# Kernel tuning notes

Hardware: AMD Instinct MI355X
Metric: run time of the kernel (lower is better)

Reference implementation:

```python
import jax, jax.numpy as jnp
import numpy as np

NUM_HEADS = 16
NUM_KV_HEADS = 8
HEAD_DIM = 128
SCALE = 1.0 / np.sqrt(HEAD_DIM)  # 0.08838834764831845
SEQ_LENS = [1536, 512, 1024, 1024]  # ragged packed sequences, total T=4096


def setup_inputs() -> dict:
    key = jax.random.key(0)
    k1, k2, k3 = jax.random.split(key, 3)
    T = sum(SEQ_LENS)
    q = jax.random.normal(k1, (T, NUM_HEADS * HEAD_DIM), dtype=jnp.float32)
    k = jax.random.normal(k2, (T, NUM_KV_HEADS * HEAD_DIM), dtype=jnp.float32)
    v = jax.random.normal(k3, (T, NUM_KV_HEADS * HEAD_DIM), dtype=jnp.float32)
    # positions restart at 0 for each packed sequence; jumps mark boundaries
    positions = jnp.asarray(np.concatenate([np.arange(L) for L in SEQ_LENS]), dtype=jnp.int32)
    return {"q": q, "k": k, "v": v, "positions": positions}


def reference(q, k, v, positions):
    T = q.shape[0]
    G = NUM_HEADS // NUM_KV_HEADS  # GQA group size
    qh = q.reshape(T, NUM_KV_HEADS, G, HEAD_DIM)
    kh = k.reshape(T, NUM_KV_HEADS, HEAD_DIM)
    vh = v.reshape(T, NUM_KV_HEADS, HEAD_DIM)
    # segment ids from position jumps (positions[i] != positions[i-1] + 1)
    jump = jnp.concatenate([
        jnp.zeros((1,), jnp.int32),
        (positions[1:] != positions[:-1] + 1).astype(jnp.int32),
    ])
    seg = jnp.cumsum(jump)  # [T]
    idx = jnp.arange(T)
    # attend only within the same packed sequence, causally
    mask = (seg[:, None] == seg[None, :]) & (idx[:, None] >= idx[None, :])  # [T, T]
    # scores: [kv_head, group, T_q, T_k]
    scores = jnp.einsum('tkgd,skd->kgts', qh, kh) * jnp.float32(SCALE)
    scores = jnp.where(mask[None, None], scores, jnp.float32(-1e30))
    p = jax.nn.softmax(scores, axis=-1)
    o = jnp.einsum('kgts,skd->tkgd', p, vh)
    return o.reshape(T, NUM_HEADS * HEAD_DIM)
```

## Files before the change

kernel.cpp:

```cpp
#include <hip/hip_runtime.h>
#include <cstdint>
#include <cstddef>

#define NUM_KV   8
#define GQA      2
#define HD       128
#define QSTRIDE  2048
#define KSTRIDE  1024
#define SCALE_LOG2E 0.12751741032075463f

typedef float    f32x4  __attribute__((ext_vector_type(4)));
typedef float    f32x2  __attribute__((ext_vector_type(2)));
typedef float    f32x16 __attribute__((ext_vector_type(16)));
typedef unsigned u32x4  __attribute__((ext_vector_type(4)));
typedef __bf16   bf16x8 __attribute__((ext_vector_type(8)));
typedef __bf16   bf16x2 __attribute__((ext_vector_type(2)));

union U8 { unsigned short u[8]; unsigned d[4]; u32x4 q; bf16x8 v; };

__device__ __forceinline__ unsigned short f2b(float f) {
    union { float f; unsigned u; } x;
    x.f = f;
    unsigned r = x.u + 0x7fffu + ((x.u >> 16) & 1u);
    return (unsigned short)(r >> 16);
}
__device__ __forceinline__ unsigned pkb(float x, float y) {
    f32x2 f = {x, y};
    bf16x2 b = __builtin_convertvector(f, bf16x2);
    union { bf16x2 b; unsigned u; } c; c.b = b;
    return c.u;
}

#define PS_STRIDE 40

__global__ __launch_bounds__(512)
void swizzle_k(const float* __restrict__ kg, unsigned short* __restrict__ Kswz,
               int T, int NT)
{
    const int tt = blockIdx.x, h = blockIdx.y;
    const int tid = threadIdx.x;
    const int c = tid >> 6, lane = tid & 63;
    const int col = lane & 31, hk = lane >> 5;
    const int row = min(tt * 32 + col, T - 1);
    const float* src = kg + (size_t)row * KSTRIDE + h * HD + c * 16 + hk * 8;
    f32x4 a = ((const f32x4*)src)[0];
    f32x4 b = ((const f32x4*)src)[1];
    u32x4 W;
    W[0] = pkb(a[0], a[1]); W[1] = pkb(a[2], a[3]);
    W[2] = pkb(b[0], b[1]); W[3] = pkb(b[2], b[3]);
    *(u32x4*)(Kswz + (((size_t)h * NT + tt) * 8 + c) * 512 + lane * 8) = W;
}

__global__ __launch_bounds__(512)
void swizzle_v(const float* __restrict__ vg, unsigned short* __restrict__ Vswz,
               int T, int NT)
{
    const int tt = blockIdx.x, h = blockIdx.y;
    const int tid = threadIdx.x;
    const int f = tid >> 6, lane = tid & 63;
    const int col = lane & 31, hk = lane >> 5;
    const int d  = (f >> 1) * 32 + col;
    const int r0 = tt * 32 + (f & 1) * 16 + hk * 8;
    float x[8];
#pragma unroll
    for (int j = 0; j < 8; ++j) {
        const int row = min(r0 + j, T - 1);
        x[j] = vg[(size_t)row * KSTRIDE + h * HD + d];
    }
    u32x4 W;
    W[0] = pkb(x[0], x[1]); W[1] = pkb(x[2], x[3]);
    W[2] = pkb(x[4], x[5]); W[3] = pkb(x[6], x[7]);
    *(u32x4*)(Vswz + (((size_t)h * NT + tt) * 8 + f) * 512 + lane * 8) = W;
}

__global__ __launch_bounds__(256, 2)
void attn_kernel(const float* __restrict__ qg, const unsigned short* __restrict__ Kswz,
                 const unsigned short* __restrict__ Vswz, const int* __restrict__ pos,
                 float* __restrict__ out, int T, int NT)
{
    __shared__ __align__(16) float Obuf[4][32 * 128];
    __shared__ float Lb[4][32];
    __shared__ __align__(16) unsigned short Ps[4][32 * PS_STRIDE];

    const int tid  = threadIdx.x;
    const int w    = tid >> 6;
    const int lane = tid & 63;
    const int col  = lane & 31;
    const int hk   = lane >> 5;

    const int bid = blockIdx.x;
    const int kvh = bid & 7;
    const int g   = (bid >> 3) & 1;
    const int qtr = bid >> 4;
    const int nq  = (T + 31) >> 5;
    const int qt  = nq - 1 - qtr;
    const int row0 = qt * 32;
    if (row0 >= T) return;
    const int hq = kvh * GQA + g;

    const int kend = min(row0 + 32, T);
    const int k_lo = row0 - pos[row0];

    const int rbase = row0 + 4 * hk;
    int rstart[16];
#pragma unroll
    for (int r = 0; r < 16; ++r) {
        const int rg = rbase + (r & 3) + 8 * (r >> 2);
        const int rc = min(rg, T - 1);
        rstart[r] = rc - pos[rc];
    }
    int rs_max = rstart[0];
#pragma unroll
    for (int r = 1; r < 16; ++r) rs_max = max(rs_max, rstart[r]);
    rs_max = max(rs_max, __shfl_xor(rs_max, 32));

    bf16x8 qf[8];
    {
        const int qr = min(row0 + col, T - 1);
        const float* qp = qg + (size_t)qr * QSTRIDE + hq * HD + hk * 8;
#pragma unroll
        for (int c = 0; c < 8; ++c) {
            f32x4 f0 = ((const f32x4*)(qp + c * 16))[0];
            f32x4 f1 = ((const f32x4*)(qp + c * 16))[1];
            U8 u;
            u.d[0] = pkb(f0[0] * SCALE_LOG2E, f0[1] * SCALE_LOG2E);
            u.d[1] = pkb(f0[2] * SCALE_LOG2E, f0[3] * SCALE_LOG2E);
            u.d[2] = pkb(f1[0] * SCALE_LOG2E, f1[1] * SCALE_LOG2E);
            u.d[3] = pkb(f1[2] * SCALE_LOG2E, f1[3] * SCALE_LOG2E);
            qf[c] = u.v;
        }
    }

    f32x16 acc[4];
#pragma unroll
    for (int nt = 0; nt < 4; ++nt)
#pragma unroll
        for (int r = 0; r < 16; ++r) acc[nt][r] = 0.f;
    float l_vec[16];
#pragma unroll
    for (int r = 0; r < 16; ++r) l_vec[r] = 0.f;

    const int t_lo = k_lo >> 5;
    const int t_hi = (kend + 31) >> 5;
    const unsigned short* kb_base = Kswz + (size_t)kvh * NT * 4096;
    const unsigned short* vb_base = Vswz + (size_t)kvh * NT * 4096;

    U8 kf[8], kfn[8], vf[8];
    int tt = t_lo + w;
    if (tt < t_hi) {
        const unsigned short* kp = kb_base + (size_t)tt * 4096 + lane * 8;
#pragma unroll
        for (int c = 0; c < 8; ++c) kf[c].q = *(const u32x4*)(kp + c * 512);
    }

    for (; tt < t_hi; tt += 4) {
        const int ttn = tt + 4;
        if (ttn < t_hi) {
            const unsigned short* kp = kb_base + (size_t)ttn * 4096 + lane * 8;
#pragma unroll
            for (int c = 0; c < 8; ++c) kfn[c].q = *(const u32x4*)(kp + c * 512);
        }
        {
            const unsigned short* vp = vb_base + (size_t)tt * 4096 + lane * 8;
#pragma unroll
            for (int f = 0; f < 8; ++f) vf[f].q = *(const u32x4*)(vp + f * 512);
        }

        f32x16 s;
#pragma unroll
        for (int r = 0; r < 16; ++r) s[r] = 0.f;
#pragma unroll
        for (int c = 0; c < 8; ++c)
            s = __builtin_amdgcn_mfma_f32_32x32x16_bf16(qf[c], kf[c].v, s, 0, 0, 0);

        const int kb  = tt * 32;
        const int key = kb + col;
        float p[16];
        if (kb >= rs_max && kb + 32 <= row0 + 1) {
#pragma unroll
            for (int r = 0; r < 16; ++r) { p[r] = exp2f(s[r]); l_vec[r] += p[r]; }
        } else {
#pragma unroll
            for (int r = 0; r < 16; ++r) {
                const int rg = rbase + (r & 3) + 8 * (r >> 2);
                const float x = (key >= rstart[r] && key <= rg) ? s[r] : -3e38f;
                p[r] = exp2f(x);
                l_vec[r] += p[r];
            }
        }

        unsigned short* Pw = (unsigned short*)Ps[w];
#pragma unroll
        for (int r = 0; r < 16; ++r)
            Pw[((r & 3) + 8 * (r >> 2) + 4 * hk) * PS_STRIDE + col] = f2b(p[r]);
        U8 pa0, pa1;
        pa0.q = *(const u32x4*)&Pw[col * PS_STRIDE + hk * 8];
        pa1.q = *(const u32x4*)&Pw[col * PS_STRIDE + 16 + hk * 8];

#pragma unroll
        for (int nt = 0; nt < 4; ++nt) {
            acc[nt] = __builtin_amdgcn_mfma_f32_32x32x16_bf16(pa0.v, vf[nt * 2].v,     acc[nt], 0, 0, 0);
            acc[nt] = __builtin_amdgcn_mfma_f32_32x32x16_bf16(pa1.v, vf[nt * 2 + 1].v, acc[nt], 0, 0, 0);
        }
#pragma unroll
        for (int c = 0; c < 8; ++c) kf[c] = kfn[c];
    }

#pragma unroll
    for (int r = 0; r < 16; ++r) {
        float sl = l_vec[r];
        sl += __shfl_xor(sl, 1);
        sl += __shfl_xor(sl, 2);
        sl += __shfl_xor(sl, 4);
        sl += __shfl_xor(sl, 8);
        sl += __shfl_xor(sl, 16);
        if (col == 0) Lb[w][(r & 3) + 8 * (r >> 2) + 4 * hk] = sl;
    }
#pragma unroll
    for (int nt = 0; nt < 4; ++nt)
#pragma unroll
        for (int r = 0; r < 16; ++r)
            Obuf[w][((r & 3) + 8 * (r >> 2) + 4 * hk) * 128 + nt * 32 + col] = acc[nt][r];

    __syncthreads();

    const int orow = tid >> 3;
    const int oc   = (tid & 7) * 16;
    const int rg   = row0 + orow;
    const float lsum = Lb[0][orow] + Lb[1][orow] + Lb[2][orow] + Lb[3][orow];
    const float inv  = (lsum > 0.f) ? (1.0f / lsum) : 0.f;
    if (rg < T) {
        float* op = out + (size_t)rg * QSTRIDE + hq * HD + oc;
#pragma unroll
        for (int j = 0; j < 4; ++j) {
            f32x4 sv = *(const f32x4*)&Obuf[0][orow * 128 + oc + j * 4];
#pragma unroll
            for (int ww = 1; ww < 4; ++ww) {
                f32x4 t = *(const f32x4*)&Obuf[ww][orow * 128 + oc + j * 4];
                sv[0] += t[0]; sv[1] += t[1]; sv[2] += t[2]; sv[3] += t[3];
            }
            sv[0] *= inv; sv[1] *= inv; sv[2] *= inv; sv[3] *= inv;
            *(f32x4*)(op + j * 4) = sv;
        }
    }
}

extern "C" void kernel_launch(void* const* d_in, const int* in_sizes, int n_in,
                              void* d_out, int out_size, void* d_ws, size_t ws_size,
                              hipStream_t stream) {
    const float* q   = (const float*)d_in[0];
    const float* k   = (const float*)d_in[1];
    const float* v   = (const float*)d_in[2];
    const int*   pos = (const int*)d_in[3];
    float* out = (float*)d_out;
    const int T  = in_sizes[0] / QSTRIDE;
    const int NT = (T + 31) / 32;

    unsigned short* Kswz = (unsigned short*)d_ws;
    unsigned short* Vswz = Kswz + (size_t)NUM_KV * NT * 4096;

    swizzle_k<<<dim3(NT, NUM_KV), 512, 0, stream>>>(k, Kswz, T, NT);
    swizzle_v<<<dim3(NT, NUM_KV), 512, 0, stream>>>(v, Vswz, T, NT);

    attn_kernel<<<dim3(NT * 16), 256, 0, stream>>>(q, Kswz, Vswz, pos, out, T, NT);
}
```

Baseline: 170.2 us.

## Fuse K/V swizzle kernels, compute S transposed, shuffle P in registers, shrink LDS

```diff
diff --git a/kernel.cpp b/kernel.cpp
--- a/kernel.cpp
+++ b/kernel.cpp
@@ -15,15 +15,10 @@
 typedef unsigned u32x4  __attribute__((ext_vector_type(4)));
 typedef __bf16   bf16x8 __attribute__((ext_vector_type(8)));
 typedef __bf16   bf16x2 __attribute__((ext_vector_type(2)));
+typedef int      i32x2  __attribute__((ext_vector_type(2)));
 
 union U8 { unsigned short u[8]; unsigned d[4]; u32x4 q; bf16x8 v; };
 
-__device__ __forceinline__ unsigned short f2b(float f) {
-    union { float f; unsigned u; } x;
-    x.f = f;
-    unsigned r = x.u + 0x7fffu + ((x.u >> 16) & 1u);
-    return (unsigned short)(r >> 16);
-}
 __device__ __forceinline__ unsigned pkb(float x, float y) {
     f32x2 f = {x, y};
     bf16x2 b = __builtin_convertvector(f, bf16x2);
@@ -31,56 +26,56 @@
     return c.u;
 }
 
-#define PS_STRIDE 40
+__device__ __forceinline__ void pl32swap(unsigned &a, unsigned &b) {
+    i32x2 r = __builtin_amdgcn_permlane32_swap((int)a, (int)b, false, false);
+    a = (unsigned)r[0];
+    b = (unsigned)r[1];
+}
 
 __global__ __launch_bounds__(512)
-void swizzle_k(const float* __restrict__ kg, unsigned short* __restrict__ Kswz,
-               int T, int NT)
-{
-    const int tt = blockIdx.x, h = blockIdx.y;
-    const int tid = threadIdx.x;
-    const int c = tid >> 6, lane = tid & 63;
-    const int col = lane & 31, hk = lane >> 5;
-    const int row = min(tt * 32 + col, T - 1);
-    const float* src = kg + (size_t)row * KSTRIDE + h * HD + c * 16 + hk * 8;
-    f32x4 a = ((const f32x4*)src)[0];
-    f32x4 b = ((const f32x4*)src)[1];
-    u32x4 W;
-    W[0] = pkb(a[0], a[1]); W[1] = pkb(a[2], a[3]);
-    W[2] = pkb(b[0], b[1]); W[3] = pkb(b[2], b[3]);
-    *(u32x4*)(Kswz + (((size_t)h * NT + tt) * 8 + c) * 512 + lane * 8) = W;
-}
-
-__global__ __launch_bounds__(512)
-void swizzle_v(const float* __restrict__ vg, unsigned short* __restrict__ Vswz,
-               int T, int NT)
+void swizzle_kv(const float* __restrict__ kg, const float* __restrict__ vg,
+                unsigned short* __restrict__ Kswz, unsigned short* __restrict__ Vswz,
+                int T, int NT)
 {
     const int tt = blockIdx.x, h = blockIdx.y;
     const int tid = threadIdx.x;
     const int f = tid >> 6, lane = tid & 63;
     const int col = lane & 31, hk = lane >> 5;
-    const int d  = (f >> 1) * 32 + col;
-    const int r0 = tt * 32 + (f & 1) * 16 + hk * 8;
-    float x[8];
-#pragma unroll
-    for (int j = 0; j < 8; ++j) {
-        const int row = min(r0 + j, T - 1);
-        x[j] = vg[(size_t)row * KSTRIDE + h * HD + d];
-    }
-    u32x4 W;
-    W[0] = pkb(x[0], x[1]); W[1] = pkb(x[2], x[3]);
-    W[2] = pkb(x[4], x[5]); W[3] = pkb(x[6], x[7]);
-    *(u32x4*)(Vswz + (((size_t)h * NT + tt) * 8 + f) * 512 + lane * 8) = W;
-}
-
-__global__ __launch_bounds__(256, 2)
+
+    if (blockIdx.z == 0) {
+        const int row = min(tt * 32 + col, T - 1);
+        const float* src = kg + (size_t)row * KSTRIDE + h * HD + f * 16 + hk * 8;
+        f32x4 a = ((const f32x4*)src)[0];
+        f32x4 b = ((const f32x4*)src)[1];
+        u32x4 W;
+        W[0] = pkb(a[0], a[1]); W[1] = pkb(a[2], a[3]);
+        W[2] = pkb(b[0], b[1]); W[3] = pkb(b[2], b[3]);
+        *(u32x4*)(Kswz + (((size_t)h * NT + tt) * 8 + f) * 512 + lane * 8) = W;
+    } else {
+        const int d  = (f >> 1) * 32 + col;
+        const int r0 = tt * 32 + (f & 1) * 16 + hk * 8;
+        float x[8];
+#pragma unroll
+        for (int j = 0; j < 8; ++j) {
+            const int row = min(r0 + j, T - 1);
+            x[j] = vg[(size_t)row * KSTRIDE + h * HD + d];
+        }
+        u32x4 W;
+        W[0] = pkb(x[0], x[1]); W[1] = pkb(x[2], x[3]);
+        W[2] = pkb(x[4], x[5]); W[3] = pkb(x[6], x[7]);
+        *(u32x4*)(Vswz + (((size_t)h * NT + tt) * 8 + f) * 512 + lane * 8) = W;
+    }
+}
+
+#define OB_STRIDE 132
+
+__global__ __launch_bounds__(256, 4)
 void attn_kernel(const float* __restrict__ qg, const unsigned short* __restrict__ Kswz,
                  const unsigned short* __restrict__ Vswz, const int* __restrict__ pos,
                  float* __restrict__ out, int T, int NT)
 {
-    __shared__ __align__(16) float Obuf[4][32 * 128];
-    __shared__ float Lb[4][32];
-    __shared__ __align__(16) unsigned short Ps[4][32 * PS_STRIDE];
+    __shared__ __align__(16) float Obuf[32 * OB_STRIDE];
+    __shared__ float Lb[32];
 
     const int tid  = threadIdx.x;
     const int w    = tid >> 6;
@@ -98,21 +93,21 @@
     if (row0 >= T) return;
     const int hq = kvh * GQA + g;
 
+    for (int i = tid; i < 32 * OB_STRIDE; i += 256) Obuf[i] = 0.f;
+    if (tid < 32) Lb[tid] = 0.f;
+    __syncthreads();
+
     const int kend = min(row0 + 32, T);
     const int k_lo = row0 - pos[row0];
 
-    const int rbase = row0 + 4 * hk;
-    int rstart[16];
-#pragma unroll
-    for (int r = 0; r < 16; ++r) {
-        const int rg = rbase + (r & 3) + 8 * (r >> 2);
-        const int rc = min(rg, T - 1);
-        rstart[r] = rc - pos[rc];
-    }
-    int rs_max = rstart[0];
-#pragma unroll
-    for (int r = 1; r < 16; ++r) rs_max = max(rs_max, rstart[r]);
-    rs_max = max(rs_max, __shfl_xor(rs_max, 32));
+    const int qrow   = min(row0 + col, T - 1);
+    const int rstart = qrow - pos[qrow];
+    int rs_max = rstart;
+    rs_max = max(rs_max, __shfl_xor(rs_max, 1));
+    rs_max = max(rs_max, __shfl_xor(rs_max, 2));
+    rs_max = max(rs_max, __shfl_xor(rs_max, 4));
+    rs_max = max(rs_max, __shfl_xor(rs_max, 8));
+    rs_max = max(rs_max, __shfl_xor(rs_max, 16));
 
     bf16x8 qf[8];
     {
@@ -136,9 +131,7 @@
     for (int nt = 0; nt < 4; ++nt)
 #pragma unroll
         for (int r = 0; r < 16; ++r) acc[nt][r] = 0.f;
-    float l_vec[16];
-#pragma unroll
-    for (int r = 0; r < 16; ++r) l_vec[r] = 0.f;
+    float l_lane = 0.f;
 
     const int t_lo = k_lo >> 5;
     const int t_hi = (kend + 31) >> 5;
@@ -169,76 +162,72 @@
         f32x16 s;
 #pragma unroll
         for (int r = 0; r < 16; ++r) s[r] = 0.f;
+        __builtin_amdgcn_s_setprio(1);
 #pragma unroll
         for (int c = 0; c < 8; ++c)
-            s = __builtin_amdgcn_mfma_f32_32x32x16_bf16(qf[c], kf[c].v, s, 0, 0, 0);
-
-        const int kb  = tt * 32;
-        const int key = kb + col;
+            s = __builtin_amdgcn_mfma_f32_32x32x16_bf16(kf[c].v, qf[c], s, 0, 0, 0);
+        __builtin_amdgcn_s_setprio(0);
+
+        const int kb = tt * 32;
         float p[16];
         if (kb >= rs_max && kb + 32 <= row0 + 1) {
 #pragma unroll
-            for (int r = 0; r < 16; ++r) { p[r] = exp2f(s[r]); l_vec[r] += p[r]; }
+            for (int r = 0; r < 16; ++r) { p[r] = exp2f(s[r]); l_lane += p[r]; }
         } else {
 #pragma unroll
             for (int r = 0; r < 16; ++r) {
-                const int rg = rbase + (r & 3) + 8 * (r >> 2);
-                const float x = (key >= rstart[r] && key <= rg) ? s[r] : -3e38f;
+                const int key = kb + (r & 3) + 8 * (r >> 2) + 4 * hk;
+                const float x = (key >= rstart && key <= qrow) ? s[r] : -3e38f;
                 p[r] = exp2f(x);
-                l_vec[r] += p[r];
+                l_lane += p[r];
             }
         }
 
-        unsigned short* Pw = (unsigned short*)Ps[w];
-#pragma unroll
-        for (int r = 0; r < 16; ++r)
-            Pw[((r & 3) + 8 * (r >> 2) + 4 * hk) * PS_STRIDE + col] = f2b(p[r]);
+        unsigned a0 = pkb(p[0],  p[1]),  a1 = pkb(p[2],  p[3]);
+        unsigned b0 = pkb(p[4],  p[5]),  b1 = pkb(p[6],  p[7]);
+        pl32swap(a0, b0); pl32swap(a1, b1);
+        unsigned c0 = pkb(p[8],  p[9]),  c1 = pkb(p[10], p[11]);
+        unsigned d0 = pkb(p[12], p[13]), d1 = pkb(p[14], p[15]);
+        pl32swap(c0, d0); pl32swap(c1, d1);
         U8 pa0, pa1;
-        pa0.q = *(const u32x4*)&Pw[col * PS_STRIDE + hk * 8];
-        pa1.q = *(const u32x4*)&Pw[col * PS_STRIDE + 16 + hk * 8];
-
+        pa0.d[0] = a0; pa0.d[1] = a1; pa0.d[2] = b0; pa0.d[3] = b1;
+        pa1.d[0] = c0; pa1.d[1] = c1; pa1.d[2] = d0; pa1.d[3] = d1;
+
+        __builtin_amdgcn_s_setprio(1);
 #pragma unroll
         for (int nt = 0; nt < 4; ++nt) {
             acc[nt] = __builtin_amdgcn_mfma_f32_32x32x16_bf16(pa0.v, vf[nt * 2].v,     acc[nt], 0, 0, 0);
             acc[nt] = __builtin_amdgcn_mfma_f32_32x32x16_bf16(pa1.v, vf[nt * 2 + 1].v, acc[nt], 0, 0, 0);
         }
+        __builtin_amdgcn_s_setprio(0);
+
 #pragma unroll
         for (int c = 0; c < 8; ++c) kf[c] = kfn[c];
     }
 
-#pragma unroll
-    for (int r = 0; r < 16; ++r) {
-        float sl = l_vec[r];
-        sl += __shfl_xor(sl, 1);
-        sl += __shfl_xor(sl, 2);
-        sl += __shfl_xor(sl, 4);
-        sl += __shfl_xor(sl, 8);
-        sl += __shfl_xor(sl, 16);
-        if (col == 0) Lb[w][(r & 3) + 8 * (r >> 2) + 4 * hk] = sl;
+    {
+        const float ls = l_lane + __shfl_xor(l_lane, 32);
+        if (hk == 0) atomicAdd(&Lb[col], ls);
     }
 #pragma unroll
     for (int nt = 0; nt < 4; ++nt)
 #pragma unroll
         for (int r = 0; r < 16; ++r)
-            Obuf[w][((r & 3) + 8 * (r >> 2) + 4 * hk) * 128 + nt * 32 + col] = acc[nt][r];
+            atomicAdd(&Obuf[((r & 3) + 8 * (r >> 2) + 4 * hk) * OB_STRIDE + nt * 32 + col],
+                      acc[nt][r]);
 
     __syncthreads();
 
     const int orow = tid >> 3;
     const int oc   = (tid & 7) * 16;
     const int rg   = row0 + orow;
-    const float lsum = Lb[0][orow] + Lb[1][orow] + Lb[2][orow] + Lb[3][orow];
+    const float lsum = Lb[orow];
     const float inv  = (lsum > 0.f) ? (1.0f / lsum) : 0.f;
     if (rg < T) {
         float* op = out + (size_t)rg * QSTRIDE + hq * HD + oc;
 #pragma unroll
         for (int j = 0; j < 4; ++j) {
-            f32x4 sv = *(const f32x4*)&Obuf[0][orow * 128 + oc + j * 4];
-#pragma unroll
-            for (int ww = 1; ww < 4; ++ww) {
-                f32x4 t = *(const f32x4*)&Obuf[ww][orow * 128 + oc + j * 4];
-                sv[0] += t[0]; sv[1] += t[1]; sv[2] += t[2]; sv[3] += t[3];
-            }
+            f32x4 sv = *(const f32x4*)&Obuf[orow * OB_STRIDE + oc + j * 4];
             sv[0] *= inv; sv[1] *= inv; sv[2] *= inv; sv[3] *= inv;
             *(f32x4*)(op + j * 4) = sv;
         }
@@ -259,8 +248,6 @@
     unsigned short* Kswz = (unsigned short*)d_ws;
     unsigned short* Vswz = Kswz + (size_t)NUM_KV * NT * 4096;
 
-    swizzle_k<<<dim3(NT, NUM_KV), 512, 0, stream>>>(k, Kswz, T, NT);
-    swizzle_v<<<dim3(NT, NUM_KV), 512, 0, stream>>>(v, Vswz, T, NT);
-
+    swizzle_kv<<<dim3(NT, NUM_KV, 2), 512, 0, stream>>>(k, v, Kswz, Vswz, T, NT);
     attn_kernel<<<dim3(NT * 16), 256, 0, stream>>>(q, Kswz, Vswz, pos, out, T, NT);
 }
```

Result: slower. 453.4 us (+166.4%).
